# Kernel tuning notes

Hardware: AMD Instinct MI355X
Metric: run time of the kernel (lower is better)

## Reference

```python
import jax, jax.numpy as jnp
import numpy as np

NUM_LAYERS = 8
HIDDEN = 128
BATCH = 262144
SKIP_CONNECTION = True
BIAS_ENABLED = True


def setup_inputs() -> dict:
    key = jax.random.key(0)
    kx, kw, kb = jax.random.split(key, 3)
    x = jax.random.normal(kx, (BATCH, HIDDEN), dtype=jnp.float32)
    # scale weights ~ 1/sqrt(fan_in) so activations stay O(1) across 8 layers
    w = jax.random.normal(kw, (NUM_LAYERS, HIDDEN, HIDDEN), dtype=jnp.float32) * (1.0 / np.sqrt(HIDDEN))
    b = jax.random.normal(kb, (NUM_LAYERS, HIDDEN), dtype=jnp.float32) * 0.01
    return {"x": x, "w": w, "b": b}


def reference(x, w, b):
    # Fused elastic MLP, full-width (active_neurons == hidden for every layer).
    # Per the Triton forward kernel: every layer (including the last) applies
    # ReLU, and with skip_connection the input block is added AFTER the
    # activation for layers > 0.
    h = x
    for layer in range(NUM_LAYERS):
        h = jax.nn.relu(jnp.einsum('bi,ji->bj', h, w[layer]) + (b[layer] if BIAS_ENABLED else 0.0))
        if SKIP_CONNECTION and layer > 0:
            h = h + x  # input_dim == hidden, skip-add over full width
    return h
```

## Files before the change

kernel.cpp:

```cpp
#include <hip/hip_runtime.h>
#include <hip/hip_bf16.h>


typedef __bf16 bf16_t;
typedef __bf16 bf16x8 __attribute__((ext_vector_type(8)));
typedef __bf16 bf16x4 __attribute__((ext_vector_type(4)));
typedef float floatx4 __attribute__((ext_vector_type(4)));

#define HID 128
#define NLAYERS 8
#define TM 64
#define LDH 136

__global__ __launch_bounds__(256) void wconv_kernel(const float* __restrict__ w,
                                                    bf16_t* __restrict__ wb) {
    int i = (blockIdx.x * 256 + threadIdx.x) * 4;
    floatx4 v = *(const floatx4*)&w[i];
    bf16x4 o = { (bf16_t)v[0], (bf16_t)v[1], (bf16_t)v[2], (bf16_t)v[3] };
    *(bf16x4*)&wb[i] = o;
}

__global__ __launch_bounds__(256, 3) void mlp_kernel(
    const float* __restrict__ x, const bf16_t* __restrict__ wb,
    const float* __restrict__ bias, float* __restrict__ out)
{
    __shared__ __align__(16) bf16_t hs[TM][LDH];
    __shared__ __align__(16) bf16_t wsh[HID][LDH];

    const int tid  = threadIdx.x;
    const int wave = tid >> 6;
    const int lane = tid & 63;
    const int c16  = lane & 15;
    const int quad = lane >> 4;
    const int m0 = (wave >> 1) * 64;
    const int n0 = (wave & 1) * 32;
    const long rowbase = (long)blockIdx.x * TM;
    const int jb = m0 + quad * 4;

    floatx4 xr[4][2];
#pragma unroll
    for (int ni = 0; ni < 2; ++ni) {
        const float* xrow = x + (rowbase + n0 + ni*16 + c16) * HID;
#pragma unroll
        for (int mi = 0; mi < 4; ++mi)
            xr[mi][ni] = *(const floatx4*)&xrow[jb + mi*16];
    }
#pragma unroll
    for (int ni = 0; ni < 2; ++ni) {
        bf16_t* hrow = &hs[n0 + ni*16 + c16][0];
#pragma unroll
        for (int mi = 0; mi < 4; ++mi) {
            floatx4 v = xr[mi][ni];
            bf16x4 o = { (bf16_t)v[0], (bf16_t)v[1], (bf16_t)v[2], (bf16_t)v[3] };
            *(bf16x4*)&hrow[jb + mi*16] = o;
        }
    }

    const bf16x8* wbv = (const bf16x8*)wb;
    bf16x8 wreg[8];
#pragma unroll
    for (int p = 0; p < 8; ++p) wreg[p] = wbv[p*256 + tid];
    floatx4 bnext[4];
#pragma unroll
    for (int mi = 0; mi < 4; ++mi) bnext[mi] = *(const floatx4*)&bias[jb + mi*16];

    for (int l = 0; l < NLAYERS; ++l) {
#pragma unroll
        for (int p = 0; p < 8; ++p) {
            int f = p*256 + tid;
            *(bf16x8*)&wsh[f >> 4][(f & 15) * 8] = wreg[p];
        }
        __syncthreads();

        floatx4 acc[4][2];
#pragma unroll
        for (int mi = 0; mi < 4; ++mi)
#pragma unroll
          for (int ni = 0; ni < 2; ++ni)
            acc[mi][ni] = bnext[mi];

        if (l + 1 < NLAYERS) {
#pragma unroll
            for (int p = 0; p < 8; ++p) wreg[p] = wbv[(l+1)*2048 + p*256 + tid];
#pragma unroll
            for (int mi = 0; mi < 4; ++mi)
                bnext[mi] = *(const floatx4*)&bias[(l+1)*HID + jb + mi*16];
        }

#pragma unroll
        for (int k = 0; k < 4; ++k) {
            const int kc = k*32 + quad*8;
            bf16x8 af[4], bfr[2];
#pragma unroll
            for (int mi = 0; mi < 4; ++mi)
                af[mi] = *(const bf16x8*)&wsh[m0 + mi*16 + c16][kc];
#pragma unroll
            for (int ni = 0; ni < 2; ++ni)
                bfr[ni] = *(const bf16x8*)&hs[n0 + ni*16 + c16][kc];
#pragma unroll
            for (int mi = 0; mi < 4; ++mi)
#pragma unroll
              for (int ni = 0; ni < 2; ++ni)
                acc[mi][ni] = __builtin_amdgcn_mfma_f32_16x16x32_bf16(
                                  af[mi], bfr[ni], acc[mi][ni], 0, 0, 0);
        }
        __syncthreads();

        if (l < NLAYERS - 1) {
#pragma unroll
            for (int ni = 0; ni < 2; ++ni) {
                bf16_t* hrow = &hs[n0 + ni*16 + c16][0];
#pragma unroll
                for (int mi = 0; mi < 4; ++mi) {
                    floatx4 v = acc[mi][ni];
                    float s0 = fmaxf(v[0], 0.0f), s1 = fmaxf(v[1], 0.0f);
                    float s2 = fmaxf(v[2], 0.0f), s3 = fmaxf(v[3], 0.0f);
                    if (l > 0) {
                        floatx4 xv = xr[mi][ni];
                        s0 += xv[0]; s1 += xv[1]; s2 += xv[2]; s3 += xv[3];
                    }
                    bf16x4 o = { (bf16_t)s0, (bf16_t)s1, (bf16_t)s2, (bf16_t)s3 };
                    *(bf16x4*)&hrow[jb + mi*16] = o;
                }
            }
        } else {
#pragma unroll
            for (int ni = 0; ni < 2; ++ni) {
                float* orow = out + (rowbase + n0 + ni*16 + c16) * HID;
#pragma unroll
                for (int mi = 0; mi < 4; ++mi) {
                    floatx4 v = acc[mi][ni];
                    floatx4 xv = xr[mi][ni];
                    floatx4 o;
                    o[0] = fmaxf(v[0], 0.0f) + xv[0];
                    o[1] = fmaxf(v[1], 0.0f) + xv[1];
                    o[2] = fmaxf(v[2], 0.0f) + xv[2];
                    o[3] = fmaxf(v[3], 0.0f) + xv[3];
                    *(floatx4*)&orow[jb + mi*16] = o;
                }
            }
        }
    }
}

extern "C" void kernel_launch(void* const* d_in, const int* in_sizes, int n_in,
                              void* d_out, int out_size, void* d_ws, size_t ws_size,
                              hipStream_t stream) {
    const float* x = (const float*)d_in[0];
    const float* w = (const float*)d_in[1];
    const float* b = (const float*)d_in[2];
    float* out = (float*)d_out;
    bf16_t* wb = (bf16_t*)d_ws;

    wconv_kernel<<<NLAYERS*HID*HID/(256*4), 256, 0, stream>>>(w, wb);

    const int nblocks = 262144 / TM;
    mlp_kernel<<<nblocks, 256, 0, stream>>>(x, wb, b, out);
}
```

Before: 291.5 us.

## Pre-swizzle bf16 weights into MFMA fragment order and load via global_load_lds

The weight-conversion kernel now writes bf16 weights already permuted into the per-lane MFMA A-fragment order. The MLP kernel uses global_load_lds to stream each layer's weights straight into LDS instead of staging them through registers. This removes the per-thread weight registers and the explicit LDS store loop, which eases register pressure. The LDS weight buffer is no longer padded, which may change bank behaviour. The next layer's weight load is issued after the compute barrier and overlapped with the activation writeback, at the cost of less prefetch lead time than the old register prefetch and a barrier before the next layer can start.

```diff
diff --git a/kernel.cpp b/kernel.cpp
--- a/kernel.cpp
+++ b/kernel.cpp
@@ -12,12 +12,25 @@
 #define TM 64
 #define LDH 136
 
+#define GLOAD_LDS16(g, l)  __builtin_amdgcn_global_load_lds(                 \
+    (__attribute__((address_space(1))) void*)(g),                            \
+    (__attribute__((address_space(3))) void*)(l), 16, 0, 0)
+
 __global__ __launch_bounds__(256) void wconv_kernel(const float* __restrict__ w,
                                                     bf16_t* __restrict__ wb) {
-    int i = (blockIdx.x * 256 + threadIdx.x) * 4;
-    floatx4 v = *(const floatx4*)&w[i];
-    bf16x4 o = { (bf16_t)v[0], (bf16_t)v[1], (bf16_t)v[2], (bf16_t)v[3] };
-    *(bf16x4*)&wb[i] = o;
+    int t = blockIdx.x * 256 + threadIdx.x;
+    int lane = t & 63;
+    int f    = (t >> 6) & 31;
+    int l    = t >> 11;
+    int H  = f >> 4, k = (f >> 2) & 3, mi = f & 3;
+    int row = H*64 + mi*16 + (lane & 15);
+    int col = k*32 + (lane >> 4) * 8;
+    const float* src = w + ((l*HID + row)*HID + col);
+    floatx4 v0 = *(const floatx4*)src;
+    floatx4 v1 = *(const floatx4*)(src + 4);
+    bf16x8 o = { (bf16_t)v0[0], (bf16_t)v0[1], (bf16_t)v0[2], (bf16_t)v0[3],
+                 (bf16_t)v1[0], (bf16_t)v1[1], (bf16_t)v1[2], (bf16_t)v1[3] };
+    *(bf16x8*)(wb + (long)t * 8) = o;
 }
 
 __global__ __launch_bounds__(256, 3) void mlp_kernel(
@@ -25,7 +38,7 @@
     const float* __restrict__ bias, float* __restrict__ out)
 {
     __shared__ __align__(16) bf16_t hs[TM][LDH];
-    __shared__ __align__(16) bf16_t wsh[HID][LDH];
+    __shared__ __align__(16) bf16_t wsh[HID*HID];
 
     const int tid  = threadIdx.x;
     const int wave = tid >> 6;
@@ -33,9 +46,16 @@
     const int c16  = lane & 15;
     const int quad = lane >> 4;
     const int m0 = (wave >> 1) * 64;
+    const int H  = wave >> 1;
     const int n0 = (wave & 1) * 32;
     const long rowbase = (long)blockIdx.x * TM;
     const int jb = m0 + quad * 4;
+
+#pragma unroll
+    for (int p = 0; p < 8; ++p) {
+        const bf16_t* src = wb + (long)(p*256 + wave*64 + lane) * 8;
+        GLOAD_LDS16(src, &wsh[(p*256 + wave*64) * 8]);
+    }
 
     floatx4 xr[4][2];
 #pragma unroll
@@ -56,22 +76,13 @@
         }
     }
 
-    const bf16x8* wbv = (const bf16x8*)wb;
-    bf16x8 wreg[8];
-#pragma unroll
-    for (int p = 0; p < 8; ++p) wreg[p] = wbv[p*256 + tid];
     floatx4 bnext[4];
 #pragma unroll
     for (int mi = 0; mi < 4; ++mi) bnext[mi] = *(const floatx4*)&bias[jb + mi*16];
 
+    __syncthreads();
+
     for (int l = 0; l < NLAYERS; ++l) {
-#pragma unroll
-        for (int p = 0; p < 8; ++p) {
-            int f = p*256 + tid;
-            *(bf16x8*)&wsh[f >> 4][(f & 15) * 8] = wreg[p];
-        }
-        __syncthreads();
-
         floatx4 acc[4][2];
 #pragma unroll
         for (int mi = 0; mi < 4; ++mi)
@@ -80,8 +91,6 @@
             acc[mi][ni] = bnext[mi];
 
         if (l + 1 < NLAYERS) {
-#pragma unroll
-            for (int p = 0; p < 8; ++p) wreg[p] = wbv[(l+1)*2048 + p*256 + tid];
 #pragma unroll
             for (int mi = 0; mi < 4; ++mi)
                 bnext[mi] = *(const floatx4*)&bias[(l+1)*HID + jb + mi*16];
@@ -93,7 +102,7 @@
             bf16x8 af[4], bfr[2];
 #pragma unroll
             for (int mi = 0; mi < 4; ++mi)
-                af[mi] = *(const bf16x8*)&wsh[m0 + mi*16 + c16][kc];
+                af[mi] = *(const bf16x8*)&wsh[((H*16 + k*4 + mi)*64 + lane) * 8];
 #pragma unroll
             for (int ni = 0; ni < 2; ++ni)
                 bfr[ni] = *(const bf16x8*)&hs[n0 + ni*16 + c16][kc];
@@ -107,6 +116,11 @@
         __syncthreads();
 
         if (l < NLAYERS - 1) {
+#pragma unroll
+            for (int p = 0; p < 8; ++p) {
+                const bf16_t* src = wb + (long)((l+1)*2048 + p*256 + wave*64 + lane) * 8;
+                GLOAD_LDS16(src, &wsh[(p*256 + wave*64) * 8]);
+            }
 #pragma unroll
             for (int ni = 0; ni < 2; ++ni) {
                 bf16_t* hrow = &hs[n0 + ni*16 + c16][0];
@@ -123,6 +137,7 @@
                     *(bf16x4*)&hrow[jb + mi*16] = o;
                 }
             }
+            __syncthreads();
         } else {
 #pragma unroll
             for (int ni = 0; ni < 2; ++ni) {
@@ -152,7 +167,7 @@
     float* out = (float*)d_out;
     bf16_t* wb = (bf16_t*)d_ws;
 
-    wconv_kernel<<<NLAYERS*HID*HID/(256*4), 256, 0, stream>>>(w, wb);
+    wconv_kernel<<<NLAYERS*HID*HID/(256*8), 256, 0, stream>>>(w, wb);
 
     const int nblocks = 262144 / TM;
     mlp_kernel<<<nblocks, 256, 0, stream>>>(x, wb, b, out);
```

After: 284.3 us. 1.03x faster.
